# Optimization experiments

Hardware: AMD Instinct MI355X
Metric: run time of the kernel (lower is better)

The kernel has to match this reference:

```python
import jax, jax.numpy as jnp
import numpy as np

L, B, H, DH, D, DFF, V = 16, 4, 20, 64, 1280, 5120, 8000
HIST, TENC, S, MAXSEQ = 1024, 512, 1, 1152


def _ln(x, w, b, eps=1e-5):
    m = x.mean(-1, keepdims=True)
    var = ((x - m) ** 2).mean(-1, keepdims=True)
    return (x - m) * jax.lax.rsqrt(var + eps) * w + b


def setup_inputs() -> dict:
    key = jax.random.key(0)
    ks = iter(jax.random.split(key, 64))
    W = 0.05  # weight init scale to keep softmax logits in a sane range
    def nrm(shape, s=W):
        return jax.random.normal(next(ks), shape, dtype=jnp.float32) * s
    return {
        # per-layer caches, stacked on a leading layer axis
        'self_k_cache': jax.random.normal(next(ks), (L, B, H, DH, HIST), jnp.float32),
        'self_v_cache': jax.random.normal(next(ks), (L, B, H, HIST, DH), jnp.float32),
        'cross_k': jax.random.normal(next(ks), (L, B, H, DH, TENC), jnp.float32) * 0.2,
        'cross_v': jax.random.normal(next(ks), (L, B, H, TENC, DH), jnp.float32),
        'input_ids': jax.random.randint(next(ks), (B, S), 0, V, dtype=jnp.int64),
        'history_len': HIST,   # python int -> static under jit
        'ids_len': S,          # python int -> static under jit
        'mask_flag': jnp.zeros((1,), jnp.float32),  # 0 during cached decode (mask row slice only valid at prefill)
        # learned parameters (emb pre-scaled by decoder.scale at export time)
        'emb': nrm((V, D), 1.0),
        'pe': nrm((1, MAXSEQ, D), 0.05),
        'snw': jnp.ones((L, D), jnp.float32), 'snb': jnp.zeros((L, D), jnp.float32),
        'wq': nrm((L, H, D, DH)), 'bq': nrm((L, H, 1, DH)),
        'wk': nrm((L, H, D, DH)),
        'wv': nrm((L, H, D, DH)), 'bv': nrm((L, H, 1, DH)),
        'fcw': nrm((L, H, DH, D)), 'fcb': nrm((L, D)),
        'cnw': jnp.ones((L, D), jnp.float32), 'cnb': jnp.zeros((L, D), jnp.float32),
        'cwq': nrm((L, H, D, DH)), 'cbq': nrm((L, H, 1, DH)),
        'cfcw': nrm((L, H, DH, D)), 'cfcb': nrm((L, D)),
        'mnw': jnp.ones((L, D), jnp.float32), 'mnb': jnp.zeros((L, D), jnp.float32),
        'w1': nrm((L, D, DFF)), 'b1': jnp.zeros((L, DFF), jnp.float32),
        'w2': nrm((L, DFF, D)), 'b2': jnp.zeros((L, D), jnp.float32),
        'lnow': jnp.ones((D,), jnp.float32), 'lnob': jnp.zeros((D,), jnp.float32),
        'proj_w': nrm((D, V)), 'proj_b': jnp.zeros((V,), jnp.float32),
    }


def reference(self_k_cache, self_v_cache, cross_k, cross_v, input_ids, history_len,
              ids_len, mask_flag, emb, pe, snw, snb, wq, bq, wk, wv, bv, fcw, fcb,
              cnw, cnb, cwq, cbq, cfcw, cfcb, mnw, mnb, w1, b1, w2, b2,
              lnow, lnob, proj_w, proj_b):
    kv = history_len + ids_len
    # token embedding (pre-scaled) + positional encoding slice
    x = emb[input_ids] + pe[:, history_len:kv]                       # [B,S,D]
    mask = (1.0 - jnp.tril(jnp.ones((ids_len, kv), jnp.float32))) * (-128.0) * mask_flag
    x = x[:, None]                                                   # [B,1,S,D]
    new_k, new_v = [], []
    for l in range(L):
        xn = _ln(x, snw[l], snb[l])
        q = jnp.matmul(xn, wq[l]) + bq[l]                            # [B,H,S,DH]
        k = jnp.swapaxes(jnp.matmul(xn, wk[l]), -1, -2)              # [B,H,DH,S] (no K bias, as in source)
        v = jnp.matmul(xn, wv[l]) + bv[l]                            # [B,H,S,DH]
        k = jnp.concatenate([self_k_cache[l], k], axis=-1)           # [B,H,DH,kv]
        v = jnp.concatenate([self_v_cache[l], v], axis=-2)           # [B,H,kv,DH]
        new_k.append(k); new_v.append(v)
        attn = jnp.matmul(jax.nn.softmax(jnp.matmul(q, k) + mask, axis=-1), v)  # [B,H,S,DH]
        x = x + jnp.matmul(attn, fcw[l]).sum(axis=1, keepdims=True) + fcb[l]
        q2 = jnp.matmul(_ln(x, cnw[l], cnb[l]), cwq[l]) + cbq[l]     # [B,H,S,DH]
        a2 = jnp.matmul(jax.nn.softmax(jnp.matmul(q2, cross_k[l]), axis=-1), cross_v[l])
        x = x + jnp.matmul(a2, cfcw[l]).sum(axis=1, keepdims=True) + cfcb[l]
        xm = _ln(x, mnw[l], mnb[l])
        x = x + jnp.matmul(jax.nn.relu(jnp.matmul(xm, w1[l]) + b1[l]), w2[l]) + b2[l]
    h = _ln(x[:, 0, -1], lnow, lnob)                                 # [B,D]
    logits = jnp.matmul(h, proj_w) + proj_b                          # [B,V]
    return (jnp.stack(new_k), jnp.stack(new_v), logits, kv)
```

## Files before the change

### kernel.cpp

```cpp
#include <hip/hip_runtime.h>

#define BB 4
#define HH 20
#define DHD 64
#define DD 1280
#define DFFN 5120
#define VV 8000
#define HIST 1024
#define TENC 512
#define KVLEN 1025
#define NLAYER 16

static const size_t NK_OFF = 0;
static const size_t NV_OFF = 83968000ull;
static const size_t LG_OFF = 167936000ull;
static const size_t KV_IDX = 167968000ull;

__device__ __forceinline__ void fma4(float4& a, float s, const float4& w) {
    a.x += s * w.x; a.y += s * w.y; a.z += s * w.z; a.w += s * w.w;
}


__global__ __launch_bounds__(256) void embed_kernel(
    const float* __restrict__ emb, const float* __restrict__ pe,
    const int* __restrict__ ids, float* __restrict__ x) {
    int i = blockIdx.x * 256 + threadIdx.x;
    if (i >= BB * DD) return;
    int b = i / DD, d = i % DD;
    int tok = ids[b];
    x[i] = emb[(size_t)tok * DD + d] + pe[(size_t)HIST * DD + d];
}

__global__ __launch_bounds__(256) void ln_fin(
    float* __restrict__ x, const float* __restrict__ pin, int np,
    const float* __restrict__ rbias,
    const float* __restrict__ lw, const float* __restrict__ lb,
    float* __restrict__ xn) {
    int b = blockIdx.x, tid = threadIdx.x;
    __shared__ float vbuf[DD];
    __shared__ float red[256];
    float* xb = x + b * DD;
    for (int i = tid; i < DD; i += 256) {
        float v = xb[i];
        if (rbias) v += rbias[i];
        for (int j = 0; j < np; ++j) v += pin[(size_t)(j * BB + b) * DD + i];
        xb[i] = v;
        vbuf[i] = v;
    }
    __syncthreads();
    float s = 0.f;
    for (int i = tid; i < DD; i += 256) s += vbuf[i];
    red[tid] = s; __syncthreads();
    for (int st = 128; st > 0; st >>= 1) { if (tid < st) red[tid] += red[tid + st]; __syncthreads(); }
    float mean = red[0] / DD; __syncthreads();
    float vs = 0.f;
    for (int i = tid; i < DD; i += 256) { float d = vbuf[i] - mean; vs += d * d; }
    red[tid] = vs; __syncthreads();
    for (int st = 128; st > 0; st >>= 1) { if (tid < st) red[tid] += red[tid + st]; __syncthreads(); }
    float rstd = rsqrtf(red[0] / DD + 1e-5f);
    for (int i = tid; i < DD; i += 256)
        xn[b * DD + i] = (vbuf[i] - mean) * rstd * lw[i] + lb[i];
}

__global__ __launch_bounds__(256) void qkv_part_k(
    const float* __restrict__ w0, const float* __restrict__ w1p, const float* __restrict__ w2p,
    const float* __restrict__ xn, float* __restrict__ outp) {
    int h = blockIdx.x;
    int mat = blockIdx.y >> 2, rc = blockIdx.y & 3;
    const float* W = (mat == 0 ? w0 : mat == 1 ? w1p : w2p) + (size_t)h * DD * DHD;
    int tid = threadIdx.x;
    int sg = tid >> 4;
    int cq = (tid & 15) * 4;
    __shared__ float acts[BB * 320];
    __shared__ float red[16][BB][64];
    int row0 = rc * 320;
    for (int i = tid; i < BB * 320; i += 256) {
        int b = i / 320, r = i % 320;
        acts[i] = xn[b * DD + row0 + r];
    }
    __syncthreads();
    float4 a0 = {0,0,0,0}, a1 = {0,0,0,0}, a2 = {0,0,0,0}, a3 = {0,0,0,0};
    const float* Wp = W + (size_t)row0 * DHD + cq;
#pragma unroll 4
    for (int it = 0; it < 20; ++it) {
        int r = sg + it * 16;
        float4 w4 = *(const float4*)(Wp + (size_t)r * DHD);
        fma4(a0, acts[r], w4);
        fma4(a1, acts[320 + r], w4);
        fma4(a2, acts[640 + r], w4);
        fma4(a3, acts[960 + r], w4);
    }
    red[sg][0][cq+0]=a0.x; red[sg][0][cq+1]=a0.y; red[sg][0][cq+2]=a0.z; red[sg][0][cq+3]=a0.w;
    red[sg][1][cq+0]=a1.x; red[sg][1][cq+1]=a1.y; red[sg][1][cq+2]=a1.z; red[sg][1][cq+3]=a1.w;
    red[sg][2][cq+0]=a2.x; red[sg][2][cq+1]=a2.y; red[sg][2][cq+2]=a2.z; red[sg][2][cq+3]=a2.w;
    red[sg][3][cq+0]=a3.x; red[sg][3][cq+1]=a3.y; red[sg][3][cq+2]=a3.z; red[sg][3][cq+3]=a3.w;
    __syncthreads();
    int b = tid >> 6, dh = tid & 63;
    float v = 0.f;
#pragma unroll
    for (int g = 0; g < 16; ++g) v += red[g][b][dh];
    outp[(size_t)(((mat * 4 + rc) * HH + h) * BB + b) * 64 + dh] = v;
}

__global__ __launch_bounds__(256) void attn_self_A(
    const float* __restrict__ kc, const float* __restrict__ vc,
    const float* __restrict__ qkvp, const float* __restrict__ bq_l,
    const float* __restrict__ bv_l, const float* __restrict__ mflagp,
    float* __restrict__ nk, float* __restrict__ nv, float* __restrict__ stats) {
    int h = blockIdx.x, b = blockIdx.y, c = blockIdx.z;
    int tid = threadIdx.x;
    __shared__ float qs[64], knS[64], vnS[64];
    __shared__ float sc4[4][256];
    __shared__ float parr[256];
    __shared__ float red[256];
    __shared__ float pvred[16][64];
    __shared__ float snS;
    float flag = mflagp[0];
    if (tid < 64) {
        float qv = bq_l[h * 64 + tid];
#pragma unroll
        for (int rc = 0; rc < 4; ++rc) qv += qkvp[(size_t)((rc * HH + h) * BB + b) * 64 + tid];
        qs[tid] = qv;
    } else if (tid < 128) {
        int l2 = tid - 64;
        float kn = 0.f;
#pragma unroll
        for (int rc = 0; rc < 4; ++rc) kn += qkvp[(size_t)(((4 + rc) * HH + h) * BB + b) * 64 + l2];
        knS[l2] = kn;
        if (c == 0) nk[(size_t)((b * HH + h) * 64 + l2) * KVLEN + HIST] = kn;
    } else if (tid < 192) {
        int l2 = tid - 128;
        float vn = bv_l[h * 64 + l2];
#pragma unroll
        for (int rc = 0; rc < 4; ++rc) vn += qkvp[(size_t)(((8 + rc) * HH + h) * BB + b) * 64 + l2];
        vnS[l2] = vn;
        if (c == 0) nv[(size_t)(b * HH + h) * KVLEN * 64 + (size_t)HIST * 64 + l2] = vn;
    }
    __syncthreads();
    int g = tid >> 6, t = tid & 63;
    int j0 = c * 256 + t * 4;
    const float* kb = kc + (size_t)(b * HH + h) * 64 * HIST;
    float* nkb = nk + (size_t)(b * HH + h) * 64 * KVLEN;
    float ax = 0, ay = 0, az = 0, aw = 0;
#pragma unroll 4
    for (int it = 0; it < 16; ++it) {
        int dh = g * 16 + it;
        float4 k4 = *(const float4*)(kb + (size_t)dh * HIST + j0);
        float* nr = nkb + (size_t)dh * KVLEN + j0;
        nr[0] = k4.x; nr[1] = k4.y; nr[2] = k4.z; nr[3] = k4.w;
        float qd = qs[dh];
        ax += qd * k4.x; ay += qd * k4.y; az += qd * k4.z; aw += qd * k4.w;
    }
    sc4[g][t*4+0] = ax; sc4[g][t*4+1] = ay; sc4[g][t*4+2] = az; sc4[g][t*4+3] = aw;
    __syncthreads();
    int j = c * 256 + tid;
    float s = sc4[0][tid] + sc4[1][tid] + sc4[2][tid] + sc4[3][tid];
    if (j != 0) s += -128.0f * flag;
    if (c == 0 && tid < 64) {
        float pp = qs[tid] * knS[tid];
#pragma unroll
        for (int off = 32; off > 0; off >>= 1) pp += __shfl_xor(pp, off, 64);
        if (tid == 0) snS = pp + (-128.0f * flag);
    }
    red[tid] = s; __syncthreads();
    for (int st = 128; st > 0; st >>= 1) { if (tid < st) red[tid] = fmaxf(red[tid], red[tid + st]); __syncthreads(); }
    float m = red[0];
    if (c == 0) m = fmaxf(m, snS);
    __syncthreads();
    float p = expf(s - m);
    parr[tid] = p; red[tid] = p; __syncthreads();
    for (int st = 128; st > 0; st >>= 1) { if (tid < st) red[tid] += red[tid + st]; __syncthreads(); }
    float ssum = red[0];
    float en = (c == 0) ? expf(snS - m) : 0.0f;
    int rg = tid >> 4, dq = (tid & 15) * 4;
    const float* vb = vc + (size_t)(b * HH + h) * HIST * 64;
    float* nvb = nv + (size_t)(b * HH + h) * KVLEN * 64;
    float vx = 0, vy = 0, vz = 0, vw = 0;
#pragma unroll 4
    for (int it = 0; it < 16; ++it) {
        int i = rg + it * 16;
        size_t jj = (size_t)(c * 256 + i);
        float4 v4 = *(const float4*)(vb + jj * 64 + dq);
        *(float4*)(nvb + jj * 64 + dq) = v4;
        float pw = parr[i];
        vx += pw * v4.x; vy += pw * v4.y; vz += pw * v4.z; vw += pw * v4.w;
    }
    pvred[rg][dq+0] = vx; pvred[rg][dq+1] = vy; pvred[rg][dq+2] = vz; pvred[rg][dq+3] = vw;
    __syncthreads();
    float* st_ = stats + (size_t)((b * HH + h) * 4 + c) * 66;
    if (tid == 0) { st_[0] = m; st_[1] = ssum + en; }
    if (tid < 64) {
        float pv = 0.f;
#pragma unroll
        for (int rgi = 0; rgi < 16; ++rgi) pv += pvred[rgi][tid];
        if (c == 0) pv += en * vnS[tid];
        st_[2 + tid] = pv;
    }
}

__global__ __launch_bounds__(256) void attn_cross_A(
    const float* __restrict__ ck, const float* __restrict__ cv,
    const float* __restrict__ qkvp, const float* __restrict__ cbq_l,
    float* __restrict__ stats) {
    int h = blockIdx.x, b = blockIdx.y, c = blockIdx.z;
    int tid = threadIdx.x;
    __shared__ float qs[64];
    __shared__ float sc4[4][256];
    __shared__ float parr[256];
    __shared__ float red[256];
    __shared__ float pvred[16][64];
    if (tid < 64) {
        float qv = cbq_l[h * 64 + tid];
#pragma unroll
        for (int rc = 0; rc < 4; ++rc) qv += qkvp[(size_t)((rc * HH + h) * BB + b) * 64 + tid];
        qs[tid] = qv;
    }
    __syncthreads();
    int g = tid >> 6, t = tid & 63;
    int j0 = c * 256 + t * 4;
    const float* kb = ck + (size_t)(b * HH + h) * 64 * TENC;
    float ax = 0, ay = 0, az = 0, aw = 0;
#pragma unroll 4
    for (int it = 0; it < 16; ++it) {
        int dh = g * 16 + it;
        float4 k4 = *(const float4*)(kb + (size_t)dh * TENC + j0);
        float qd = qs[dh];
        ax += qd * k4.x; ay += qd * k4.y; az += qd * k4.z; aw += qd * k4.w;
    }
    sc4[g][t*4+0] = ax; sc4[g][t*4+1] = ay; sc4[g][t*4+2] = az; sc4[g][t*4+3] = aw;
    __syncthreads();
    float s = sc4[0][tid] + sc4[1][tid] + sc4[2][tid] + sc4[3][tid];
    red[tid] = s; __syncthreads();
    for (int st = 128; st > 0; st >>= 1) { if (tid < st) red[tid] = fmaxf(red[tid], red[tid + st]); __syncthreads(); }
    float m = red[0]; __syncthreads();
    float p = expf(s - m);
    parr[tid] = p; red[tid] = p; __syncthreads();
    for (int st = 128; st > 0; st >>= 1) { if (tid < st) red[tid] += red[tid + st]; __syncthreads(); }
    float ssum = red[0];
    int rg = tid >> 4, dq = (tid & 15) * 4;
    const float* vb = cv + (size_t)(b * HH + h) * TENC * 64;
    float vx = 0, vy = 0, vz = 0, vw = 0;
#pragma unroll 4
    for (int it = 0; it < 16; ++it) {
        int i = rg + it * 16;
        size_t jj = (size_t)(c * 256 + i);
        float4 v4 = *(const float4*)(vb + jj * 64 + dq);
        float pw = parr[i];
        vx += pw * v4.x; vy += pw * v4.y; vz += pw * v4.z; vw += pw * v4.w;
    }
    pvred[rg][dq+0] = vx; pvred[rg][dq+1] = vy; pvred[rg][dq+2] = vz; pvred[rg][dq+3] = vw;
    __syncthreads();
    float* st_ = stats + (size_t)((b * HH + h) * 4 + c) * 66;
    if (tid == 0) { st_[0] = m; st_[1] = ssum; }
    if (tid < 64) {
        float pv = 0.f;
#pragma unroll
        for (int rgi = 0; rgi < 16; ++rgi) pv += pvred[rgi][tid];
        st_[2 + tid] = pv;
    }
}

template <int ACT_MODE>
__global__ __launch_bounds__(256) void gemv_part(
    const float* __restrict__ W, int ldw, int K, int N,
    const float* __restrict__ actbuf, const float* __restrict__ abias,
    const float* __restrict__ pin, int np,
    const float* __restrict__ stats, int nc,
    float* __restrict__ outp) {
    int cc = blockIdx.x, rc = blockIdx.y, R = gridDim.y, tid = threadIdx.x;
    int rows = K / R, row0 = rc * rows;
    int sg = tid >> 6, t = tid & 63;
    __shared__ float acts[BB * 320];
    __shared__ float red[4][BB][256];
    for (int i = tid; i < BB * rows; i += 256) {
        int b = i / rows, r = i % rows;
        float v;
        if (ACT_MODE == 0) {
            v = actbuf[(size_t)b * K + row0 + r];
        } else if (ACT_MODE == 1) {
            v = abias[row0 + r];
            for (int j = 0; j < np; ++j) v += pin[(size_t)(j * BB + b) * K + row0 + r];
            v = fmaxf(v, 0.0f);
        } else {
            int gr = row0 + r;
            int hh = gr >> 6, dh = gr & 63;
            const float* st = stats + (size_t)((b * HH + hh) * 4) * 66;
            float M = st[0];
            for (int cI = 1; cI < nc; ++cI) M = fmaxf(M, st[cI * 66]);
            float den = 0.f, num = 0.f;
            for (int cI = 0; cI < nc; ++cI) {
                float e = expf(st[cI * 66] - M);
                den += e * st[cI * 66 + 1];
                num += e * st[cI * 66 + 2 + dh];
            }
            v = num / den;
        }
        acts[b * rows + r] = v;
    }
    __syncthreads();
    int col = cc * 256 + t * 4;
    float4 a0 = {0,0,0,0}, a1 = {0,0,0,0}, a2 = {0,0,0,0}, a3 = {0,0,0,0};
    if (col < N) {
        const float* Wp = W + (size_t)row0 * ldw + col;
#pragma unroll 4
        for (int r = sg; r < rows; r += 4) {
            float4 w4 = *(const float4*)(Wp + (size_t)r * ldw);
            fma4(a0, acts[r], w4);
            fma4(a1, acts[rows + r], w4);
            fma4(a2, acts[2 * rows + r], w4);
            fma4(a3, acts[3 * rows + r], w4);
        }
    }
    red[sg][0][t*4+0]=a0.x; red[sg][0][t*4+1]=a0.y; red[sg][0][t*4+2]=a0.z; red[sg][0][t*4+3]=a0.w;
    red[sg][1][t*4+0]=a1.x; red[sg][1][t*4+1]=a1.y; red[sg][1][t*4+2]=a1.z; red[sg][1][t*4+3]=a1.w;
    red[sg][2][t*4+0]=a2.x; red[sg][2][t*4+1]=a2.y; red[sg][2][t*4+2]=a2.z; red[sg][2][t*4+3]=a2.w;
    red[sg][3][t*4+0]=a3.x; red[sg][3][t*4+1]=a3.y; red[sg][3][t*4+2]=a3.z; red[sg][3][t*4+3]=a3.w;
    __syncthreads();
    int b = tid >> 6, t2 = tid & 63;
    int col2 = cc * 256 + t2 * 4;
    if (col2 < N) {
        float4 o;
        o.x = red[0][b][t2*4+0] + red[1][b][t2*4+0] + red[2][b][t2*4+0] + red[3][b][t2*4+0];
        o.y = red[0][b][t2*4+1] + red[1][b][t2*4+1] + red[2][b][t2*4+1] + red[3][b][t2*4+1];
        o.z = red[0][b][t2*4+2] + red[1][b][t2*4+2] + red[2][b][t2*4+2] + red[3][b][t2*4+2];
        o.w = red[0][b][t2*4+3] + red[1][b][t2*4+3] + red[2][b][t2*4+3] + red[3][b][t2*4+3];
        *(float4*)(outp + (size_t)(rc * BB + b) * N + col2) = o;
    }
}

__global__ __launch_bounds__(256) void proj_fin(
    const float* __restrict__ part, const float* __restrict__ pb, float* __restrict__ out) {
    int c = blockIdx.x * 256 + threadIdx.x;
    if (c < VV) {
        for (int b = 0; b < BB; ++b) {
            float v = pb[c];
            for (int rc = 0; rc < 8; ++rc) v += part[(size_t)(rc * BB + b) * VV + c];
            out[LG_OFF + (size_t)b * VV + c] = v;
        }
    }
    if (blockIdx.x == 0 && threadIdx.x == 0) out[KV_IDX] = (float)(HIST + 1);
}

extern "C" void kernel_launch(void* const* d_in, const int* in_sizes, int n_in,
                              void* d_out, int out_size, void* d_ws, size_t ws_size,
                              hipStream_t stream) {
    const float* kc    = (const float*)d_in[0];
    const float* vc    = (const float*)d_in[1];
    const float* ck    = (const float*)d_in[2];
    const float* cv    = (const float*)d_in[3];
    const int*   ids   = (const int*)d_in[4];
    const float* mflag = (const float*)d_in[7];
    const float* emb   = (const float*)d_in[8];
    const float* pe    = (const float*)d_in[9];
    const float* snw   = (const float*)d_in[10];
    const float* snb   = (const float*)d_in[11];
    const float* wq    = (const float*)d_in[12];
    const float* bq    = (const float*)d_in[13];
    const float* wk    = (const float*)d_in[14];
    const float* wv    = (const float*)d_in[15];
    const float* bv    = (const float*)d_in[16];
    const float* fcw   = (const float*)d_in[17];
    const float* fcb   = (const float*)d_in[18];
    const float* cnw   = (const float*)d_in[19];
    const float* cnb   = (const float*)d_in[20];
    const float* cwq   = (const float*)d_in[21];
    const float* cbq   = (const float*)d_in[22];
    const float* cfcw  = (const float*)d_in[23];
    const float* cfcb  = (const float*)d_in[24];
    const float* mnw   = (const float*)d_in[25];
    const float* mnb   = (const float*)d_in[26];
    const float* w1    = (const float*)d_in[27];
    const float* b1    = (const float*)d_in[28];
    const float* w2    = (const float*)d_in[29];
    const float* b2    = (const float*)d_in[30];
    const float* lnow  = (const float*)d_in[31];
    const float* lnob  = (const float*)d_in[32];
    const float* projw = (const float*)d_in[33];
    const float* projb = (const float*)d_in[34];

    float* out = (float*)d_out;
    float* ws  = (float*)d_ws;

    float* x     = ws;
    float* xn    = ws + 5120;
    float* qkvp  = ws + 10240;
    float* stats = ws + 71680;
    float* part1 = ws + 92800;
    float* part2 = ws + 420480;

    float* nk = out + NK_OFF;
    float* nv = out + NV_OFF;

    embed_kernel<<<20, 256, 0, stream>>>(emb, pe, ids, x);
    ln_fin<<<BB, 256, 0, stream>>>(x, nullptr, 0, nullptr, snw, snb, xn);

    for (int l = 0; l < NLAYER; ++l) {
        const float* kc_l  = kc + (size_t)l * BB * HH * DHD * HIST;
        const float* vc_l  = vc + (size_t)l * BB * HH * HIST * DHD;
        const float* ck_l  = ck + (size_t)l * BB * HH * DHD * TENC;
        const float* cv_l  = cv + (size_t)l * BB * HH * TENC * DHD;
        float* nk_l = nk + (size_t)l * BB * HH * DHD * KVLEN;
        float* nv_l = nv + (size_t)l * BB * HH * KVLEN * DHD;
        const float* wq_l   = wq + (size_t)l * HH * DD * DHD;
        const float* wk_l   = wk + (size_t)l * HH * DD * DHD;
        const float* wv_l   = wv + (size_t)l * HH * DD * DHD;
        const float* cwq_l  = cwq + (size_t)l * HH * DD * DHD;
        const float* bq_l   = bq + (size_t)l * HH * DHD;
        const float* bv_l   = bv + (size_t)l * HH * DHD;
        const float* cbq_l  = cbq + (size_t)l * HH * DHD;
        const float* fcw_l  = fcw + (size_t)l * HH * DHD * DD;
        const float* cfcw_l = cfcw + (size_t)l * HH * DHD * DD;
        const float* fcb_l  = fcb + (size_t)l * DD;
        const float* cfcb_l = cfcb + (size_t)l * DD;
        const float* w1_l   = w1 + (size_t)l * DD * DFFN;
        const float* b1_l   = b1 + (size_t)l * DFFN;
        const float* w2_l   = w2 + (size_t)l * DFFN * DD;
        const float* b2_l   = b2 + (size_t)l * DD;

        qkv_part_k<<<dim3(HH, 12), 256, 0, stream>>>(wq_l, wk_l, wv_l, xn, qkvp);
        attn_self_A<<<dim3(HH, BB, 4), 256, 0, stream>>>(kc_l, vc_l, qkvp, bq_l, bv_l, mflag, nk_l, nv_l, stats);
        gemv_part<2><<<dim3(5, 16), 256, 0, stream>>>(fcw_l, DD, DD, DD, nullptr, nullptr, nullptr, 0, stats, 4, part2);
        ln_fin<<<BB, 256, 0, stream>>>(x, part2, 16, fcb_l, cnw + l * DD, cnb + l * DD, xn);

        qkv_part_k<<<dim3(HH, 4), 256, 0, stream>>>(cwq_l, cwq_l, cwq_l, xn, qkvp);
        attn_cross_A<<<dim3(HH, BB, 2), 256, 0, stream>>>(ck_l, cv_l, qkvp, cbq_l, stats);
        gemv_part<2><<<dim3(5, 16), 256, 0, stream>>>(cfcw_l, DD, DD, DD, nullptr, nullptr, nullptr, 0, stats, 2, part2);
        ln_fin<<<BB, 256, 0, stream>>>(x, part2, 16, cfcb_l, mnw + l * DD, mnb + l * DD, xn);

        gemv_part<0><<<dim3(20, 16), 256, 0, stream>>>(w1_l, DFFN, DD, DFFN, xn, nullptr, nullptr, 0, nullptr, 0, part1);
        gemv_part<1><<<dim3(5, 16), 256, 0, stream>>>(w2_l, DD, DFFN, DD, nullptr, b1_l, part1, 16, nullptr, 0, part2);
        const float* nlw = (l < NLAYER - 1) ? snw + (l + 1) * DD : lnow;
        const float* nlb = (l < NLAYER - 1) ? snb + (l + 1) * DD : lnob;
        ln_fin<<<BB, 256, 0, stream>>>(x, part2, 16, b2_l, nlw, nlb, xn);
    }

    gemv_part<0><<<dim3(32, 8), 256, 0, stream>>>(projw, VV, DD, VV, xn, nullptr, nullptr, 0, nullptr, 0, part1);
    proj_fin<<<32, 256, 0, stream>>>(part1, projb, out);
}
```

Measured before the change: 2.957 ms.

## Fuse residual+LayerNorm into consumer GEMVs and widen attention split-K grids

Removes the standalone ln_fin kernels by having every block of the following GEMV/QKV kernel recompute the residual sum and LayerNorm into shared memory, with one block writing the new residual into a ping-pong buffer. Attention kernels split the sequence into 128-wide chunks (8 for self, 4 for cross), giving more blocks. The GEMVs move to 64-column tiles with different row splits. This cuts kernel launches and serialization, at the cost of redundant per-block LayerNorm work and reading partial sums in every block.

```diff
diff --git a/kernel.cpp b/kernel.cpp
--- a/kernel.cpp
+++ b/kernel.cpp
@@ -20,7 +20,6 @@
     a.x += s * w.x; a.y += s * w.y; a.z += s * w.z; a.w += s * w.w;
 }
 
-
 __global__ __launch_bounds__(256) void embed_kernel(
     const float* __restrict__ emb, const float* __restrict__ pe,
     const int* __restrict__ ids, float* __restrict__ x) {
@@ -31,75 +30,79 @@
     x[i] = emb[(size_t)tok * DD + d] + pe[(size_t)HIST * DD + d];
 }
 
-__global__ __launch_bounds__(256) void ln_fin(
-    float* __restrict__ x, const float* __restrict__ pin, int np,
-    const float* __restrict__ rbias,
+__device__ __forceinline__ void ln_preload(
+    const float* __restrict__ xold, const float* __restrict__ rbias,
+    const float* __restrict__ pin, int np,
     const float* __restrict__ lw, const float* __restrict__ lb,
-    float* __restrict__ xn) {
-    int b = blockIdx.x, tid = threadIdx.x;
-    __shared__ float vbuf[DD];
-    __shared__ float red[256];
-    float* xb = x + b * DD;
-    for (int i = tid; i < DD; i += 256) {
-        float v = xb[i];
-        if (rbias) v += rbias[i];
-        for (int j = 0; j < np; ++j) v += pin[(size_t)(j * BB + b) * DD + i];
-        xb[i] = v;
-        vbuf[i] = v;
-    }
-    __syncthreads();
+    float* __restrict__ xnew, bool doWrite, float (*vbuf)[DD]) {
+    int tid = threadIdx.x;
+    int w = tid >> 6, lane = tid & 63;
+    float vloc[20];
     float s = 0.f;
-    for (int i = tid; i < DD; i += 256) s += vbuf[i];
-    red[tid] = s; __syncthreads();
-    for (int st = 128; st > 0; st >>= 1) { if (tid < st) red[tid] += red[tid + st]; __syncthreads(); }
-    float mean = red[0] / DD; __syncthreads();
-    float vs = 0.f;
-    for (int i = tid; i < DD; i += 256) { float d = vbuf[i] - mean; vs += d * d; }
-    red[tid] = vs; __syncthreads();
-    for (int st = 128; st > 0; st >>= 1) { if (tid < st) red[tid] += red[tid + st]; __syncthreads(); }
-    float rstd = rsqrtf(red[0] / DD + 1e-5f);
-    for (int i = tid; i < DD; i += 256)
-        xn[b * DD + i] = (vbuf[i] - mean) * rstd * lw[i] + lb[i];
-}
-
-__global__ __launch_bounds__(256) void qkv_part_k(
+#pragma unroll
+    for (int e = 0; e < 20; ++e) {
+        int d = e * 64 + lane;
+        float v = xold[w * DD + d];
+        if (rbias) v += rbias[d];
+        for (int j = 0; j < np; ++j) v += pin[(size_t)(j * BB + w) * DD + d];
+        vloc[e] = v; s += v;
+    }
+    if (doWrite) {
+#pragma unroll
+        for (int e = 0; e < 20; ++e) xnew[w * DD + e * 64 + lane] = vloc[e];
+    }
+#pragma unroll
+    for (int off = 32; off; off >>= 1) s += __shfl_xor(s, off, 64);
+    float mean = s * (1.0f / DD);
+    float sq = 0.f;
+#pragma unroll
+    for (int e = 0; e < 20; ++e) { float d0 = vloc[e] - mean; sq += d0 * d0; }
+#pragma unroll
+    for (int off = 32; off; off >>= 1) sq += __shfl_xor(sq, off, 64);
+    float rstd = rsqrtf(sq * (1.0f / DD) + 1e-5f);
+#pragma unroll
+    for (int e = 0; e < 20; ++e) {
+        int d = e * 64 + lane;
+        vbuf[w][d] = (vloc[e] - mean) * rstd * lw[d] + lb[d];
+    }
+}
+
+__global__ __launch_bounds__(256) void qkv64(
     const float* __restrict__ w0, const float* __restrict__ w1p, const float* __restrict__ w2p,
-    const float* __restrict__ xn, float* __restrict__ outp) {
-    int h = blockIdx.x;
-    int mat = blockIdx.y >> 2, rc = blockIdx.y & 3;
+    const float* __restrict__ xold, const float* __restrict__ rbias,
+    const float* __restrict__ pin, int np,
+    const float* __restrict__ lw, const float* __restrict__ lb,
+    float* __restrict__ xnew, float* __restrict__ outp) {
+    int h = blockIdx.x, my = blockIdx.y;
+    int mat = my >> 2, rc = my & 3;
     const float* W = (mat == 0 ? w0 : mat == 1 ? w1p : w2p) + (size_t)h * DD * DHD;
-    int tid = threadIdx.x;
-    int sg = tid >> 4;
-    int cq = (tid & 15) * 4;
-    __shared__ float acts[BB * 320];
+    __shared__ float vbuf[BB][DD];
     __shared__ float red[16][BB][64];
+    ln_preload(xold, rbias, pin, np, lw, lb, xnew, (xnew != nullptr) && h == 0 && my == 0, vbuf);
+    __syncthreads();
+    int tid = threadIdx.x, cl = tid & 15, sg = tid >> 4;
     int row0 = rc * 320;
-    for (int i = tid; i < BB * 320; i += 256) {
-        int b = i / 320, r = i % 320;
-        acts[i] = xn[b * DD + row0 + r];
-    }
-    __syncthreads();
     float4 a0 = {0,0,0,0}, a1 = {0,0,0,0}, a2 = {0,0,0,0}, a3 = {0,0,0,0};
-    const float* Wp = W + (size_t)row0 * DHD + cq;
-#pragma unroll 4
+    const float* Wp = W + (size_t)row0 * DHD + cl * 4;
+#pragma unroll 5
     for (int it = 0; it < 20; ++it) {
         int r = sg + it * 16;
         float4 w4 = *(const float4*)(Wp + (size_t)r * DHD);
-        fma4(a0, acts[r], w4);
-        fma4(a1, acts[320 + r], w4);
-        fma4(a2, acts[640 + r], w4);
-        fma4(a3, acts[960 + r], w4);
-    }
+        int ai = row0 + r;
+        fma4(a0, vbuf[0][ai], w4); fma4(a1, vbuf[1][ai], w4);
+        fma4(a2, vbuf[2][ai], w4); fma4(a3, vbuf[3][ai], w4);
+    }
+    int cq = cl * 4;
     red[sg][0][cq+0]=a0.x; red[sg][0][cq+1]=a0.y; red[sg][0][cq+2]=a0.z; red[sg][0][cq+3]=a0.w;
     red[sg][1][cq+0]=a1.x; red[sg][1][cq+1]=a1.y; red[sg][1][cq+2]=a1.z; red[sg][1][cq+3]=a1.w;
     red[sg][2][cq+0]=a2.x; red[sg][2][cq+1]=a2.y; red[sg][2][cq+2]=a2.z; red[sg][2][cq+3]=a2.w;
     red[sg][3][cq+0]=a3.x; red[sg][3][cq+1]=a3.y; red[sg][3][cq+2]=a3.z; red[sg][3][cq+3]=a3.w;
     __syncthreads();
-    int b = tid >> 6, dh = tid & 63;
+    int b = tid >> 6, c = tid & 63;
     float v = 0.f;
 #pragma unroll
-    for (int g = 0; g < 16; ++g) v += red[g][b][dh];
-    outp[(size_t)(((mat * 4 + rc) * HH + h) * BB + b) * 64 + dh] = v;
+    for (int g = 0; g < 16; ++g) v += red[g][b][c];
+    outp[(size_t)((my * HH + h) * BB + b) * 64 + c] = v;
 }
 
 __global__ __launch_bounds__(256) void attn_self_A(
@@ -110,9 +113,9 @@
     int h = blockIdx.x, b = blockIdx.y, c = blockIdx.z;
     int tid = threadIdx.x;
     __shared__ float qs[64], knS[64], vnS[64];
-    __shared__ float sc4[4][256];
-    __shared__ float parr[256];
-    __shared__ float red[256];
+    __shared__ float sc8[8][128];
+    __shared__ float parr[128];
+    __shared__ float red[128];
     __shared__ float pvred[16][64];
     __shared__ float snS;
     float flag = mflagp[0];
@@ -127,7 +130,7 @@
 #pragma unroll
         for (int rc = 0; rc < 4; ++rc) kn += qkvp[(size_t)(((4 + rc) * HH + h) * BB + b) * 64 + l2];
         knS[l2] = kn;
-        if (c == 0) nk[(size_t)((b * HH + h) * 64 + l2) * KVLEN + HIST] = kn;
+        if (c == 0) nk[((size_t)(b * HH + h) * 64 + l2) * KVLEN + HIST] = kn;
     } else if (tid < 192) {
         int l2 = tid - 128;
         float vn = bv_l[h * 64 + l2];
@@ -137,57 +140,63 @@
         if (c == 0) nv[(size_t)(b * HH + h) * KVLEN * 64 + (size_t)HIST * 64 + l2] = vn;
     }
     __syncthreads();
-    int g = tid >> 6, t = tid & 63;
-    int j0 = c * 256 + t * 4;
+    int clK = tid & 31, gK = tid >> 5;
+    int jb = c * 128 + clK * 4;
     const float* kb = kc + (size_t)(b * HH + h) * 64 * HIST;
     float* nkb = nk + (size_t)(b * HH + h) * 64 * KVLEN;
     float ax = 0, ay = 0, az = 0, aw = 0;
-#pragma unroll 4
-    for (int it = 0; it < 16; ++it) {
-        int dh = g * 16 + it;
-        float4 k4 = *(const float4*)(kb + (size_t)dh * HIST + j0);
-        float* nr = nkb + (size_t)dh * KVLEN + j0;
+#pragma unroll
+    for (int it = 0; it < 8; ++it) {
+        int dh = gK * 8 + it;
+        float4 k4 = *(const float4*)(kb + (size_t)dh * HIST + jb);
+        float* nr = nkb + (size_t)dh * KVLEN + jb;
         nr[0] = k4.x; nr[1] = k4.y; nr[2] = k4.z; nr[3] = k4.w;
         float qd = qs[dh];
         ax += qd * k4.x; ay += qd * k4.y; az += qd * k4.z; aw += qd * k4.w;
     }
-    sc4[g][t*4+0] = ax; sc4[g][t*4+1] = ay; sc4[g][t*4+2] = az; sc4[g][t*4+3] = aw;
-    __syncthreads();
-    int j = c * 256 + tid;
-    float s = sc4[0][tid] + sc4[1][tid] + sc4[2][tid] + sc4[3][tid];
-    if (j != 0) s += -128.0f * flag;
+    sc8[gK][clK*4+0] = ax; sc8[gK][clK*4+1] = ay; sc8[gK][clK*4+2] = az; sc8[gK][clK*4+3] = aw;
+    __syncthreads();
+    float s = 0.f;
+    if (tid < 128) {
+#pragma unroll
+        for (int g = 0; g < 8; ++g) s += sc8[g][tid];
+        int j = c * 128 + tid;
+        if (j != 0) s += -128.0f * flag;
+    }
     if (c == 0 && tid < 64) {
         float pp = qs[tid] * knS[tid];
 #pragma unroll
-        for (int off = 32; off > 0; off >>= 1) pp += __shfl_xor(pp, off, 64);
+        for (int off = 32; off; off >>= 1) pp += __shfl_xor(pp, off, 64);
         if (tid == 0) snS = pp + (-128.0f * flag);
     }
-    red[tid] = s; __syncthreads();
-    for (int st = 128; st > 0; st >>= 1) { if (tid < st) red[tid] = fmaxf(red[tid], red[tid + st]); __syncthreads(); }
+    if (tid < 128) red[tid] = s;
+    __syncthreads();
+    for (int st = 64; st; st >>= 1) { if (tid < st) red[tid] = fmaxf(red[tid], red[tid + st]); __syncthreads(); }
     float m = red[0];
     if (c == 0) m = fmaxf(m, snS);
     __syncthreads();
-    float p = expf(s - m);
-    parr[tid] = p; red[tid] = p; __syncthreads();
-    for (int st = 128; st > 0; st >>= 1) { if (tid < st) red[tid] += red[tid + st]; __syncthreads(); }
+    float p = 0.f;
+    if (tid < 128) { p = expf(s - m); parr[tid] = p; red[tid] = p; }
+    __syncthreads();
+    for (int st = 64; st; st >>= 1) { if (tid < st) red[tid] += red[tid + st]; __syncthreads(); }
     float ssum = red[0];
     float en = (c == 0) ? expf(snS - m) : 0.0f;
-    int rg = tid >> 4, dq = (tid & 15) * 4;
+    int clV = tid & 15, rg = tid >> 4;
     const float* vb = vc + (size_t)(b * HH + h) * HIST * 64;
     float* nvb = nv + (size_t)(b * HH + h) * KVLEN * 64;
     float vx = 0, vy = 0, vz = 0, vw = 0;
-#pragma unroll 4
-    for (int it = 0; it < 16; ++it) {
-        int i = rg + it * 16;
-        size_t jj = (size_t)(c * 256 + i);
-        float4 v4 = *(const float4*)(vb + jj * 64 + dq);
-        *(float4*)(nvb + jj * 64 + dq) = v4;
+#pragma unroll
+    for (int it = 0; it < 8; ++it) {
+        int i = rg * 8 + it;
+        size_t jj = (size_t)(c * 128 + i);
+        float4 v4 = *(const float4*)(vb + jj * 64 + clV * 4);
+        *(float4*)(nvb + jj * 64 + clV * 4) = v4;
         float pw = parr[i];
         vx += pw * v4.x; vy += pw * v4.y; vz += pw * v4.z; vw += pw * v4.w;
     }
-    pvred[rg][dq+0] = vx; pvred[rg][dq+1] = vy; pvred[rg][dq+2] = vz; pvred[rg][dq+3] = vw;
-    __syncthreads();
-    float* st_ = stats + (size_t)((b * HH + h) * 4 + c) * 66;
+    pvred[rg][clV*4+0] = vx; pvred[rg][clV*4+1] = vy; pvred[rg][clV*4+2] = vz; pvred[rg][clV*4+3] = vw;
+    __syncthreads();
+    float* st_ = stats + (size_t)((b * HH + h) * 8 + c) * 66;
     if (tid == 0) { st_[0] = m; st_[1] = ssum + en; }
     if (tid < 64) {
         float pv = 0.f;
@@ -205,9 +214,9 @@
     int h = blockIdx.x, b = blockIdx.y, c = blockIdx.z;
     int tid = threadIdx.x;
     __shared__ float qs[64];
-    __shared__ float sc4[4][256];
-    __shared__ float parr[256];
-    __shared__ float red[256];
+    __shared__ float sc8[8][128];
+    __shared__ float parr[128];
+    __shared__ float red[128];
     __shared__ float pvred[16][64];
     if (tid < 64) {
         float qv = cbq_l[h * 64 + tid];
@@ -216,39 +225,46 @@
         qs[tid] = qv;
     }
     __syncthreads();
-    int g = tid >> 6, t = tid & 63;
-    int j0 = c * 256 + t * 4;
+    int clK = tid & 31, gK = tid >> 5;
+    int jb = c * 128 + clK * 4;
     const float* kb = ck + (size_t)(b * HH + h) * 64 * TENC;
     float ax = 0, ay = 0, az = 0, aw = 0;
-#pragma unroll 4
-    for (int it = 0; it < 16; ++it) {
-        int dh = g * 16 + it;
-        float4 k4 = *(const float4*)(kb + (size_t)dh * TENC + j0);
+#pragma unroll
+    for (int it = 0; it < 8; ++it) {
+        int dh = gK * 8 + it;
+        float4 k4 = *(const float4*)(kb + (size_t)dh * TENC + jb);
         float qd = qs[dh];
         ax += qd * k4.x; ay += qd * k4.y; az += qd * k4.z; aw += qd * k4.w;
     }
-    sc4[g][t*4+0] = ax; sc4[g][t*4+1] = ay; sc4[g][t*4+2] = az; sc4[g][t*4+3] = aw;
-    __syncthreads();
-    float s = sc4[0][tid] + sc4[1][tid] + sc4[2][tid] + sc4[3][tid];
-    red[tid] = s; __syncthreads();
-    for (int st = 128; st > 0; st >>= 1) { if (tid < st) red[tid] = fmaxf(red[tid], red[tid + st]); __syncthreads(); }
-    float m = red[0]; __syncthreads();
-    float p = expf(s - m);
-    parr[tid] = p; red[tid] = p; __syncthreads();
-    for (int st = 128; st > 0; st >>= 1) { if (tid < st) red[tid] += red[tid + st]; __syncthreads(); }
+    sc8[gK][clK*4+0] = ax; sc8[gK][clK*4+1] = ay; sc8[gK][clK*4+2] = az; sc8[gK][clK*4+3] = aw;
+    __syncthreads();
+    float s = 0.f;
+    if (tid < 128) {
+#pragma unroll
+        for (int g = 0; g < 8; ++g) s += sc8[g][tid];
+    }
+    if (tid < 128) red[tid] = s;
+    __syncthreads();
+    for (int st = 64; st; st >>= 1) { if (tid < st) red[tid] = fmaxf(red[tid], red[tid + st]); __syncthreads(); }
+    float m = red[0];
+    __syncthreads();
+    float p = 0.f;
+    if (tid < 128) { p = expf(s - m); parr[tid] = p; red[tid] = p; }
+    __syncthreads();
+    for (int st = 64; st; st >>= 1) { if (tid < st) red[tid] += red[tid + st]; __syncthreads(); }
     float ssum = red[0];
-    int rg = tid >> 4, dq = (tid & 15) * 4;
+    int clV = tid & 15, rg = tid >> 4;
     const float* vb = cv + (size_t)(b * HH + h) * TENC * 64;
     float vx = 0, vy = 0, vz = 0, vw = 0;
-#pragma unroll 4
-    for (int it = 0; it < 16; ++it) {
-        int i = rg + it * 16;
-        size_t jj = (size_t)(c * 256 + i);
-        float4 v4 = *(const float4*)(vb + jj * 64 + dq);
+#pragma unroll
+    for (int it = 0; it < 8; ++it) {
+        int i = rg * 8 + it;
+        size_t jj = (size_t)(c * 128 + i);
+        float4 v4 = *(const float4*)(vb + jj * 64 + clV * 4);
         float pw = parr[i];
         vx += pw * v4.x; vy += pw * v4.y; vz += pw * v4.z; vw += pw * v4.w;
     }
-    pvred[rg][dq+0] = vx; pvred[rg][dq+1] = vy; pvred[rg][dq+2] = vz; pvred[rg][dq+3] = vw;
+    pvred[rg][clV*4+0] = vx; pvred[rg][clV*4+1] = vy; pvred[rg][clV*4+2] = vz; pvred[rg][clV*4+3] = vw;
     __syncthreads();
     float* st_ = stats + (size_t)((b * HH + h) * 4 + c) * 66;
     if (tid == 0) { st_[0] = m; st_[1] = ssum; }
@@ -260,71 +276,79 @@
     }
 }
 
-template <int ACT_MODE>
-__global__ __launch_bounds__(256) void gemv_part(
+template <int ACT>
+__global__ __launch_bounds__(256) void gemv64(
     const float* __restrict__ W, int ldw, int K, int N,
-    const float* __restrict__ actbuf, const float* __restrict__ abias,
+    const float* __restrict__ xold, const float* __restrict__ rbias,
     const float* __restrict__ pin, int np,
+    const float* __restrict__ lw, const float* __restrict__ lb,
+    float* __restrict__ xnew,
+    const float* __restrict__ abias,
     const float* __restrict__ stats, int nc,
     float* __restrict__ outp) {
     int cc = blockIdx.x, rc = blockIdx.y, R = gridDim.y, tid = threadIdx.x;
     int rows = K / R, row0 = rc * rows;
-    int sg = tid >> 6, t = tid & 63;
-    __shared__ float acts[BB * 320];
-    __shared__ float red[4][BB][256];
-    for (int i = tid; i < BB * rows; i += 256) {
-        int b = i / rows, r = i % rows;
-        float v;
-        if (ACT_MODE == 0) {
-            v = actbuf[(size_t)b * K + row0 + r];
-        } else if (ACT_MODE == 1) {
-            v = abias[row0 + r];
-            for (int j = 0; j < np; ++j) v += pin[(size_t)(j * BB + b) * K + row0 + r];
-            v = fmaxf(v, 0.0f);
+    __shared__ float vbuf[BB][DD];
+    __shared__ float red[16][BB][64];
+    float* vb = &vbuf[0][0];
+    if (ACT == 0) {
+        ln_preload(xold, rbias, pin, np, lw, lb, xnew, (xnew != nullptr) && cc == 0 && rc == 0, vbuf);
+    } else {
+        for (int i = tid; i < BB * rows; i += 256) {
+            int b = i / rows, r = i % rows;
+            float v;
+            if (ACT == 1) {
+                v = abias[row0 + r];
+                for (int j = 0; j < np; ++j) v += pin[(size_t)(j * BB + b) * K + row0 + r];
+                v = fmaxf(v, 0.0f);
+            } else {
+                int gr = row0 + r, hh = gr >> 6, dh = gr & 63;
+                const float* st = stats + (size_t)(b * HH + hh) * nc * 66;
+                float M = st[0];
+                for (int cI = 1; cI < nc; ++cI) M = fmaxf(M, st[cI * 66]);
+                float den = 0.f, num = 0.f;
+                for (int cI = 0; cI < nc; ++cI) {
+                    float e = expf(st[cI * 66] - M);
+                    den += e * st[cI * 66 + 1];
+                    num += e * st[cI * 66 + 2 + dh];
+                }
+                v = num / den;
+            }
+            vb[i] = v;
+        }
+    }
+    __syncthreads();
+    int cl = tid & 15, sg = tid >> 4;
+    int colb = cc * 64;
+    float4 a0 = {0,0,0,0}, a1 = {0,0,0,0}, a2 = {0,0,0,0}, a3 = {0,0,0,0};
+    const float* Wp = W + (size_t)row0 * ldw + colb + cl * 4;
+    int iters = rows >> 4;
+#pragma unroll 4
+    for (int it = 0; it < iters; ++it) {
+        int r = sg + it * 16;
+        float4 w4 = *(const float4*)(Wp + (size_t)r * ldw);
+        if (ACT == 0) {
+            int ai = row0 + r;
+            fma4(a0, vbuf[0][ai], w4); fma4(a1, vbuf[1][ai], w4);
+            fma4(a2, vbuf[2][ai], w4); fma4(a3, vbuf[3][ai], w4);
         } else {
-            int gr = row0 + r;
-            int hh = gr >> 6, dh = gr & 63;
-            const float* st = stats + (size_t)((b * HH + hh) * 4) * 66;
-            float M = st[0];
-            for (int cI = 1; cI < nc; ++cI) M = fmaxf(M, st[cI * 66]);
-            float den = 0.f, num = 0.f;
-            for (int cI = 0; cI < nc; ++cI) {
-                float e = expf(st[cI * 66] - M);
-                den += e * st[cI * 66 + 1];
-                num += e * st[cI * 66 + 2 + dh];
-            }
-            v = num / den;
+            fma4(a0, vb[r], w4);             fma4(a1, vb[rows + r], w4);
+            fma4(a2, vb[2 * rows + r], w4);  fma4(a3, vb[3 * rows + r], w4);
         }
-        acts[b * rows + r] = v;
-    }
-    __syncthreads();
-    int col = cc * 256 + t * 4;
-    float4 a0 = {0,0,0,0}, a1 = {0,0,0,0}, a2 = {0,0,0,0}, a3 = {0,0,0,0};
+    }
+    int cq = cl * 4;
+    red[sg][0][cq+0]=a0.x; red[sg][0][cq+1]=a0.y; red[sg][0][cq+2]=a0.z; red[sg][0][cq+3]=a0.w;
+    red[sg][1][cq+0]=a1.x; red[sg][1][cq+1]=a1.y; red[sg][1][cq+2]=a1.z; red[sg][1][cq+3]=a1.w;
+    red[sg][2][cq+0]=a2.x; red[sg][2][cq+1]=a2.y; red[sg][2][cq+2]=a2.z; red[sg][2][cq+3]=a2.w;
+    red[sg][3][cq+0]=a3.x; red[sg][3][cq+1]=a3.y; red[sg][3][cq+2]=a3.z; red[sg][3][cq+3]=a3.w;
+    __syncthreads();
+    int b = tid >> 6, c = tid & 63;
+    int col = colb + c;
     if (col < N) {
-        const float* Wp = W + (size_t)row0 * ldw + col;
-#pragma unroll 4
-        for (int r = sg; r < rows; r += 4) {
-            float4 w4 = *(const float4*)(Wp + (size_t)r * ldw);
-            fma4(a0, acts[r], w4);
-            fma4(a1, acts[rows + r], w4);
-            fma4(a2, acts[2 * rows + r], w4);
-            fma4(a3, acts[3 * rows + r], w4);
-        }
-    }
-    red[sg][0][t*4+0]=a0.x; red[sg][0][t*4+1]=a0.y; red[sg][0][t*4+2]=a0.z; red[sg][0][t*4+3]=a0.w;
-    red[sg][1][t*4+0]=a1.x; red[sg][1][t*4+1]=a1.y; red[sg][1][t*4+2]=a1.z; red[sg][1][t*4+3]=a1.w;
-    red[sg][2][t*4+0]=a2.x; red[sg][2][t*4+1]=a2.y; red[sg][2][t*4+2]=a2.z; red[sg][2][t*4+3]=a2.w;
-    red[sg][3][t*4+0]=a3.x; red[sg][3][t*4+1]=a3.y; red[sg][3][t*4+2]=a3.z; red[sg][3][t*4+3]=a3.w;
-    __syncthreads();
-    int b = tid >> 6, t2 = tid & 63;
-    int col2 = cc * 256 + t2 * 4;
-    if (col2 < N) {
-        float4 o;
-        o.x = red[0][b][t2*4+0] + red[1][b][t2*4+0] + red[2][b][t2*4+0] + red[3][b][t2*4+0];
-        o.y = red[0][b][t2*4+1] + red[1][b][t2*4+1] + red[2][b][t2*4+1] + red[3][b][t2*4+1];
-        o.z = red[0][b][t2*4+2] + red[1][b][t2*4+2] + red[2][b][t2*4+2] + red[3][b][t2*4+2];
-        o.w = red[0][b][t2*4+3] + red[1][b][t2*4+3] + red[2][b][t2*4+3] + red[3][b][t2*4+3];
-        *(float4*)(outp + (size_t)(rc * BB + b) * N + col2) = o;
+        float v = 0.f;
+#pragma unroll
+        for (int g = 0; g < 16; ++g) v += red[g][b][c];
+        outp[(size_t)(rc * BB + b) * N + col] = v;
     }
 }
 
@@ -334,7 +358,7 @@
     if (c < VV) {
         for (int b = 0; b < BB; ++b) {
             float v = pb[c];
-            for (int rc = 0; rc < 8; ++rc) v += part[(size_t)(rc * BB + b) * VV + c];
+            for (int rc = 0; rc < 4; ++rc) v += part[(size_t)(rc * BB + b) * VV + c];
             out[LG_OFF + (size_t)b * VV + c] = v;
         }
     }
@@ -381,18 +405,23 @@
     float* out = (float*)d_out;
     float* ws  = (float*)d_ws;
 
-    float* x     = ws;
-    float* xn    = ws + 5120;
-    float* qkvp  = ws + 10240;
-    float* stats = ws + 71680;
-    float* part1 = ws + 92800;
-    float* part2 = ws + 420480;
+    float* xA     = ws;
+    float* xB     = ws + 5120;
+    float* qkvp   = ws + 10240;
+    float* selfS  = ws + 71680;
+    float* crossS = ws + 113920;
+    float* fcP    = ws + 135040;
+    float* cfcP   = ws + 176000;
+    float* f1P    = ws + 216960;
+    float* ff2P   = ws + 298880;
+    float* projP  = ws + 380800;
 
     float* nk = out + NK_OFF;
     float* nv = out + NV_OFF;
 
-    embed_kernel<<<20, 256, 0, stream>>>(emb, pe, ids, x);
-    ln_fin<<<BB, 256, 0, stream>>>(x, nullptr, 0, nullptr, snw, snb, xn);
+    embed_kernel<<<20, 256, 0, stream>>>(emb, pe, ids, xA);
+    float* xo = xA;
+    float* xn2 = xB;
 
     for (int l = 0; l < NLAYER; ++l) {
         const float* kc_l  = kc + (size_t)l * BB * HH * DHD * HIST;
@@ -417,23 +446,37 @@
         const float* w2_l   = w2 + (size_t)l * DFFN * DD;
         const float* b2_l   = b2 + (size_t)l * DD;
 
-        qkv_part_k<<<dim3(HH, 12), 256, 0, stream>>>(wq_l, wk_l, wv_l, xn, qkvp);
-        attn_self_A<<<dim3(HH, BB, 4), 256, 0, stream>>>(kc_l, vc_l, qkvp, bq_l, bv_l, mflag, nk_l, nv_l, stats);
-        gemv_part<2><<<dim3(5, 16), 256, 0, stream>>>(fcw_l, DD, DD, DD, nullptr, nullptr, nullptr, 0, stats, 4, part2);
-        ln_fin<<<BB, 256, 0, stream>>>(x, part2, 16, fcb_l, cnw + l * DD, cnb + l * DD, xn);
-
-        qkv_part_k<<<dim3(HH, 4), 256, 0, stream>>>(cwq_l, cwq_l, cwq_l, xn, qkvp);
-        attn_cross_A<<<dim3(HH, BB, 2), 256, 0, stream>>>(ck_l, cv_l, qkvp, cbq_l, stats);
-        gemv_part<2><<<dim3(5, 16), 256, 0, stream>>>(cfcw_l, DD, DD, DD, nullptr, nullptr, nullptr, 0, stats, 2, part2);
-        ln_fin<<<BB, 256, 0, stream>>>(x, part2, 16, cfcb_l, mnw + l * DD, mnb + l * DD, xn);
-
-        gemv_part<0><<<dim3(20, 16), 256, 0, stream>>>(w1_l, DFFN, DD, DFFN, xn, nullptr, nullptr, 0, nullptr, 0, part1);
-        gemv_part<1><<<dim3(5, 16), 256, 0, stream>>>(w2_l, DD, DFFN, DD, nullptr, b1_l, part1, 16, nullptr, 0, part2);
-        const float* nlw = (l < NLAYER - 1) ? snw + (l + 1) * DD : lnow;
-        const float* nlb = (l < NLAYER - 1) ? snb + (l + 1) * DD : lnob;
-        ln_fin<<<BB, 256, 0, stream>>>(x, part2, 16, b2_l, nlw, nlb, xn);
-    }
-
-    gemv_part<0><<<dim3(32, 8), 256, 0, stream>>>(projw, VV, DD, VV, xn, nullptr, nullptr, 0, nullptr, 0, part1);
-    proj_fin<<<32, 256, 0, stream>>>(part1, projb, out);
-}
+        const float* qrb  = (l == 0) ? nullptr : b2 + (size_t)(l - 1) * DD;
+        const float* qpin = (l == 0) ? nullptr : ff2P;
+        int          qnp  = (l == 0) ? 0 : 16;
+        qkv64<<<dim3(HH, 12), 256, 0, stream>>>(wq_l, wk_l, wv_l, xo, qrb, qpin, qnp,
+                                                snw + l * DD, snb + l * DD, xn2, qkvp);
+        { float* t = xo; xo = xn2; xn2 = t; }
+
+        attn_self_A<<<dim3(HH, BB, 8), 256, 0, stream>>>(kc_l, vc_l, qkvp, bq_l, bv_l, mflag,
+                                                         nk_l, nv_l, selfS);
+        gemv64<2><<<dim3(20, 8), 256, 0, stream>>>(fcw_l, DD, DD, DD,
+            nullptr, nullptr, nullptr, 0, nullptr, nullptr, nullptr, nullptr, selfS, 8, fcP);
+
+        qkv64<<<dim3(HH, 4), 256, 0, stream>>>(cwq_l, cwq_l, cwq_l, xo, fcb_l, fcP, 8,
+                                               cnw + l * DD, cnb + l * DD, xn2, qkvp);
+        { float* t = xo; xo = xn2; xn2 = t; }
+
+        attn_cross_A<<<dim3(HH, BB, 4), 256, 0, stream>>>(ck_l, cv_l, qkvp, cbq_l, crossS);
+        gemv64<2><<<dim3(20, 8), 256, 0, stream>>>(cfcw_l, DD, DD, DD,
+            nullptr, nullptr, nullptr, 0, nullptr, nullptr, nullptr, nullptr, crossS, 4, cfcP);
+
+        gemv64<0><<<dim3(80, 4), 256, 0, stream>>>(w1_l, DFFN, DD, DFFN,
+            xo, cfcb_l, cfcP, 8, mnw + l * DD, mnb + l * DD, xn2,
+            nullptr, nullptr, 0, f1P);
+        { float* t = xo; xo = xn2; xn2 = t; }
+
+        gemv64<1><<<dim3(20, 16), 256, 0, stream>>>(w2_l, DD, DFFN, DD,
+            nullptr, nullptr, f1P, 4, nullptr, nullptr, nullptr, b1_l, nullptr, 0, ff2P);
+    }
+
+    gemv64<0><<<dim3(125, 4), 256, 0, stream>>>(projw, VV, DD, VV,
+        xo, b2 + (size_t)(NLAYER - 1) * DD, ff2P, 16, lnow, lnob, nullptr,
+        nullptr, nullptr, 0, projP);
+    proj_fin<<<32, 256, 0, stream>>>(projP, projb, out);
+}
```

Result: slower. 4.135 ms (+39.8%).
